# Optimization experiments

Measured on AMD Instinct MI355X. Metric: run time of the kernel, lower is better.

## Reference

```python
import jax, jax.numpy as jnp
import numpy as np

N = 100000      # nodes
E = 3200000     # edges (avg degree 32)
IN_CH = 32
EDGE_DIM = 11
HID = IN_CH + 4 + EDGE_DIM   # 47
OUT = 128


def setup_inputs() -> dict:
    key = jax.random.key(0)
    ks = jax.random.split(key, 10)
    x = jax.random.normal(ks[0], (N, IN_CH), dtype=jnp.float32)
    pos = jax.random.normal(ks[1], (N, 3), dtype=jnp.float32) * 10.0
    nrm = jax.random.normal(ks[2], (N, 3), dtype=jnp.float32)
    normal = nrm / jnp.linalg.norm(nrm, axis=1, keepdims=True)
    # edges with src != dst (avoids degenerate zero-distance point pairs)
    src = jax.random.randint(ks[3], (E,), 0, N)
    off = jax.random.randint(ks[4], (E,), 1, N)
    dst = (src + off) % N
    edge_index = jnp.stack([src, dst], axis=0).astype(jnp.int64)
    edge_attr = jax.random.normal(ks[5], (E, EDGE_DIM), dtype=jnp.float32)
    W1 = jax.random.normal(ks[6], (HID, HID), dtype=jnp.float32) / np.sqrt(HID)
    b1 = jnp.zeros((HID,), dtype=jnp.float32)
    g1 = jnp.ones((HID,), dtype=jnp.float32)
    be1 = jnp.zeros((HID,), dtype=jnp.float32)
    W2 = jax.random.normal(ks[7], (HID, OUT), dtype=jnp.float32) / np.sqrt(HID)
    b2 = jnp.zeros((OUT,), dtype=jnp.float32)
    g2 = jnp.ones((OUT,), dtype=jnp.float32)
    be2 = jnp.zeros((OUT,), dtype=jnp.float32)
    return {"x": x, "pos": pos, "normal": normal, "edge_attr": edge_attr,
            "W1": W1, "b1": b1, "g1": g1, "be1": be1,
            "W2": W2, "b2": b2, "g2": g2, "be2": be2,
            "edge_index": edge_index}


def _angle(v1, v2):
    return jnp.arctan2(jnp.linalg.norm(jnp.cross(v1, v2), axis=1),
                       jnp.sum(v1 * v2, axis=1))


def _layernorm(h, g, b, eps=1e-5):
    mu = jnp.mean(h, axis=-1, keepdims=True)
    var = jnp.var(h, axis=-1, keepdims=True)  # biased, matches torch LayerNorm
    return (h - mu) / jnp.sqrt(var + eps) * g + b


def reference(x, pos, normal, edge_attr, W1, b1, g1, be1, W2, b2, g2, be2, edge_index):
    src, dst = edge_index[0], edge_index[1]  # message flows src(j) -> dst(i)
    pos_i, pos_j = pos[dst], pos[src]
    n_i, n_j = normal[dst], normal[src]
    x_j = x[src]
    pseudo = pos_j - pos_i                                  # [E,3]
    ppf = jnp.stack([jnp.linalg.norm(pseudo, axis=1),
                     _angle(n_i, pseudo),
                     _angle(n_j, pseudo),
                     _angle(n_i, n_j)], axis=1)             # [E,4]
    msg = jnp.concatenate([x_j, ppf, edge_attr], axis=1)    # [E,47]
    # local_nn = MLP([47,47,128]): (Lin->ReLU->LayerNorm->Dropout(eval)) x2
    h = _layernorm(jax.nn.relu(msg @ W1 + b1), g1, be1)     # [E,47]
    h = _layernorm(jax.nn.relu(h @ W2 + b2), g2, be2)       # [E,128]
    out = jax.ops.segment_max(h, dst, num_segments=N)       # scatter-max per target node
    return jnp.where(jnp.isfinite(out), out, 0.0)           # nodes w/o edges -> 0
```

## Files before the change

### kernel.cpp

```cpp
#include <hip/hip_runtime.h>
#include <cstdint>
#include <cstddef>


typedef _Float16 f16x8 __attribute__((ext_vector_type(8)));
typedef _Float16 f16x2 __attribute__((ext_vector_type(2)));
typedef float    f32x4 __attribute__((ext_vector_type(4)));

#define ENC_NEGINF 0x007FFFFFu
#define LDK 64
#define LDH 132

__device__ __forceinline__ int swz(int row, int col) {
    return (col & 7) | ((((col >> 3) ^ row) & 7) << 3);
}

__device__ __forceinline__ unsigned fenc(float f) {
    unsigned u = __float_as_uint(f);
    return (u & 0x80000000u) ? ~u : (u | 0x80000000u);
}

__global__ void init_out_kernel(unsigned* __restrict__ out, int n4) {
    int i = blockIdx.x * blockDim.x + threadIdx.x;
    if (i < n4)
        ((uint4*)out)[i] = make_uint4(ENC_NEGINF, ENC_NEGINF, ENC_NEGINF, ENC_NEGINF);
}

__global__ void finalize_out_kernel(float* __restrict__ out, int n) {
    int i = blockIdx.x * blockDim.x + threadIdx.x;
    if (i < n) {
        unsigned k = __float_as_uint(out[i]);
        float r;
        if (k == ENC_NEGINF) r = 0.0f;
        else {
            unsigned u = (k & 0x80000000u) ? (k ^ 0x80000000u) : ~k;
            r = __uint_as_float(u);
        }
        out[i] = r;
    }
}

__global__ void zero_kernel(int* __restrict__ p, int n) {
    int i = blockIdx.x * blockDim.x + threadIdx.x;
    if (i < n) p[i] = 0;
}

__global__ void hist_kernel(const int* __restrict__ dstI, int* __restrict__ counts, int E) {
    int i = blockIdx.x * blockDim.x + threadIdx.x;
    if (i < E) atomicAdd(&counts[dstI[i]], 1);
}

__global__ __launch_bounds__(1024) void scan_blk(const int* __restrict__ in,
                                                 int* __restrict__ outp,
                                                 int* __restrict__ bsums, int N) {
    __shared__ int wsum[16];
    const int tid = threadIdx.x, lane = tid & 63, wid = tid >> 6;
    int i = blockIdx.x * 1024 + tid;
    int v = (i < N) ? in[i] : 0;
    int incl = v;
#pragma unroll
    for (int m = 1; m < 64; m <<= 1) {
        int t = __shfl_up(incl, m, 64);
        if (lane >= m) incl += t;
    }
    if (lane == 63) wsum[wid] = incl;
    __syncthreads();
    int woff = 0;
#pragma unroll
    for (int k = 0; k < 16; ++k) woff += (k < wid) ? wsum[k] : 0;
    if (i < N) outp[i] = woff + incl - v;
    if (tid == 1023 && bsums != nullptr) bsums[blockIdx.x] = woff + incl;
}

__global__ __launch_bounds__(1024) void scan_add(int* __restrict__ outp,
                                                 const int* __restrict__ bsums, int N) {
    int i = blockIdx.x * 1024 + threadIdx.x;
    if (i < N) outp[i] += bsums[blockIdx.x];
}

__global__ void scatter_kernel(const int* __restrict__ srcI, const int* __restrict__ dstI,
                               int* __restrict__ nextp,
                               int2* __restrict__ se, int* __restrict__ dst_g, int E) {
    int i = blockIdx.x * blockDim.x + threadIdx.x;
    if (i < E) {
        int d = dstI[i];
        int p = atomicAdd(&nextp[d], 1);
        se[p] = make_int2(srcI[i], i);
        dst_g[p] = d;
    }
}

__global__ __launch_bounds__(512, 4) void edge_kernel_csr(
    const float* __restrict__ x,   const float* __restrict__ pos,
    const float* __restrict__ nrm, const float* __restrict__ ea,
    const float* __restrict__ W1,  const float* __restrict__ b1,
    const float* __restrict__ g1,  const float* __restrict__ be1,
    const float* __restrict__ W2,  const float* __restrict__ b2,
    const float* __restrict__ g2,  const float* __restrict__ be2,
    const int2* __restrict__ se,   const int* __restrict__ dst_g,
    unsigned* __restrict__ out, int E, int ntiles, int tilesPerBlock)
{
    __shared__ _Float16 W1t[48][LDK];
    __shared__ _Float16 W2t[128][LDK];
    __shared__ _Float16 msgA[128][LDK];
    __shared__ _Float16 h2w[128][LDH];
    __shared__ int dstL[128];

    const int lane = threadIdx.x & 63;
    const int w    = threadIdx.x >> 6;
    const int c16  = lane & 15;
    const int g    = lane >> 4;
    const int row0 = w * 16;

    for (int i = threadIdx.x; i < 48 * 64; i += 512) {
        int n = i >> 6, k = i & 63;
        W1t[n][swz(n, k)] = (n < 47 && k < 47) ? (_Float16)W1[k * 47 + n] : (_Float16)0.f;
    }
    for (int i = threadIdx.x; i < 128 * 64; i += 512) {
        int n = i >> 6, k = i & 63;
        W2t[n][swz(n, k)] = (k < 47) ? (_Float16)W2[k * 128 + n] : (_Float16)0.f;
    }
    for (int i = threadIdx.x; i < 128 * LDK; i += 512)
        (&msgA[0][0])[i] = (_Float16)0.f;

    float b1v[3], g1v[3], be1v[3];
#pragma unroll
    for (int n = 0; n < 3; ++n) {
        int cc = n * 16 + c16;
        bool vld = cc < 47;
        b1v[n]  = vld ? b1[cc]  : 0.f;
        g1v[n]  = vld ? g1[cc]  : 0.f;
        be1v[n] = vld ? be1[cc] : 0.f;
    }
    float b2v[8], g2v[8], be2v[8];
#pragma unroll
    for (int n = 0; n < 8; ++n) {
        int cc = n * 16 + c16;
        b2v[n] = b2[cc]; g2v[n] = g2[cc]; be2v[n] = be2[cc];
    }
    __syncthreads();

    const int xr = lane >> 2;
    const int xc = (lane & 3) * 8;
    const int eg = lane / 11, ec = lane - eg * 11;
    const bool ea_act  = lane < 44;
    const bool geo_act = lane < 48;

    const int tbeg = blockIdx.x * tilesPerBlock;
    int tend = tbeg + tilesPerBlock;
    if (tend > ntiles) tend = ntiles;

    for (int tile = tbeg; tile < tend; ++tile) {
        const int base = tile * 128 + row0;

        {
            int p = base + xr;
            bool vx = p < E;
            int s = vx ? se[p].x : 0;
            const float4* xp = (const float4*)(x + (size_t)s * 32 + xc);
            float4 xa = xp[0];
            float4 xb = xp[1];

            float eav0 = 0.f, eav1 = 0.f, eav2 = 0.f, eav3 = 0.f;
            if (ea_act) {
                int p0 = base + 0 * 4 + eg, p1 = base + 1 * 4 + eg;
                int p2 = base + 2 * 4 + eg, p3 = base + 3 * 4 + eg;
                int e0 = (p0 < E) ? se[p0].y : 0;
                int e1 = (p1 < E) ? se[p1].y : 0;
                int e2 = (p2 < E) ? se[p2].y : 0;
                int e3 = (p3 < E) ? se[p3].y : 0;
                eav0 = (p0 < E) ? ea[(size_t)e0 * 11 + ec] : 0.f;
                eav1 = (p1 < E) ? ea[(size_t)e1 * 11 + ec] : 0.f;
                eav2 = (p2 < E) ? ea[(size_t)e2 * 11 + ec] : 0.f;
                eav3 = (p3 < E) ? ea[(size_t)e3 * 11 + ec] : 0.f;
            }

            float gpix = 0.f, gpiy = 0.f, gpiz = 0.f;
            float gpjx = 0.f, gpjy = 0.f, gpjz = 0.f;
            float gnix = 0.f, gniy = 0.f, gniz = 0.f;
            float gnjx = 0.f, gnjy = 0.f, gnjz = 0.f;
            int pd = -1;
            if (geo_act) {
                int pg = base + c16;
                bool v = pg < E;
                int s2 = v ? se[pg].x : 0;
                int d2 = v ? dst_g[pg] : 0;
                pd = v ? d2 : -1;
                gpix = pos[d2 * 3 + 0]; gpiy = pos[d2 * 3 + 1]; gpiz = pos[d2 * 3 + 2];
                gpjx = pos[s2 * 3 + 0]; gpjy = pos[s2 * 3 + 1]; gpjz = pos[s2 * 3 + 2];
                gnix = nrm[d2 * 3 + 0]; gniy = nrm[d2 * 3 + 1]; gniz = nrm[d2 * 3 + 2];
                gnjx = nrm[s2 * 3 + 0]; gnjy = nrm[s2 * 3 + 1]; gnjz = nrm[s2 * 3 + 2];
            }

            {
                int r = row0 + xr;
                f16x8 hv;
                hv[0] = (_Float16)(vx ? xa.x : 0.f); hv[1] = (_Float16)(vx ? xa.y : 0.f);
                hv[2] = (_Float16)(vx ? xa.z : 0.f); hv[3] = (_Float16)(vx ? xa.w : 0.f);
                hv[4] = (_Float16)(vx ? xb.x : 0.f); hv[5] = (_Float16)(vx ? xb.y : 0.f);
                hv[6] = (_Float16)(vx ? xb.z : 0.f); hv[7] = (_Float16)(vx ? xb.w : 0.f);
                *(f16x8*)&msgA[r][swz(r, xc)] = hv;
            }
            if (ea_act) {
                int r0 = row0 + 0 * 4 + eg; msgA[r0][swz(r0, 36 + ec)] = (_Float16)eav0;
                int r1 = row0 + 1 * 4 + eg; msgA[r1][swz(r1, 36 + ec)] = (_Float16)eav1;
                int r2 = row0 + 2 * 4 + eg; msgA[r2][swz(r2, 36 + ec)] = (_Float16)eav2;
                int r3 = row0 + 3 * 4 + eg; msgA[r3][swz(r3, 36 + ec)] = (_Float16)eav3;
            }
            if (geo_act) {
                int r = row0 + c16;
                float px = gpjx - gpix, py = gpjy - gpiy, pz = gpjz - gpiz;
                float v1x, v1y, v1z, v2x, v2y, v2z;
                if (g == 0)      { v1x = gnix; v1y = gniy; v1z = gniz; v2x = px;   v2y = py;   v2z = pz; }
                else if (g == 1) { v1x = gnjx; v1y = gnjy; v1z = gnjz; v2x = px;   v2y = py;   v2z = pz; }
                else             { v1x = gnix; v1y = gniy; v1z = gniz; v2x = gnjx; v2y = gnjy; v2z = gnjz; }
                float cx = v1y * v2z - v1z * v2y;
                float cy = v1z * v2x - v1x * v2z;
                float cz = v1x * v2y - v1y * v2x;
                float ang = atan2f(sqrtf(cx * cx + cy * cy + cz * cz),
                                   v1x * v2x + v1y * v2y + v1z * v2z);
                msgA[r][swz(r, 33 + g)] = (_Float16)ang;
                if (g == 0) {
                    msgA[r][swz(r, 32)] = (_Float16)sqrtf(px * px + py * py + pz * pz);
                    dstL[r] = pd;
                }
            }
        }

        f32x4 acc1[3];
#pragma unroll
        for (int n = 0; n < 3; ++n) acc1[n] = (f32x4){0.f, 0.f, 0.f, 0.f};
#pragma unroll
        for (int ks = 0; ks < 2; ++ks) {
            int ar = row0 + c16;
            f16x8 a = *(const f16x8*)&msgA[ar][swz(ar, ks * 32 + g * 8)];
#pragma unroll
            for (int n = 0; n < 3; ++n) {
                int br = n * 16 + c16;
                f16x8 b = *(const f16x8*)&W1t[br][swz(br, ks * 32 + g * 8)];
                acc1[n] = __builtin_amdgcn_mfma_f32_16x16x32_f16(a, b, acc1[n], 0, 0, 0);
            }
        }
#pragma unroll
        for (int q = 0; q < 4; ++q) {
            float t0 = fmaxf(acc1[0][q] + b1v[0], 0.f);
            float t1 = fmaxf(acc1[1][q] + b1v[1], 0.f);
            float t2 = fmaxf(acc1[2][q] + b1v[2], 0.f);
            float s = t0 + t1 + t2;
            float s2 = t0 * t0 + t1 * t1 + t2 * t2;
#pragma unroll
            for (int m = 1; m < 16; m <<= 1) {
                s  += __shfl_xor(s,  m, 64);
                s2 += __shfl_xor(s2, m, 64);
            }
            float mu  = s * (1.f / 47.f);
            float var = s2 * (1.f / 47.f) - mu * mu;
            float rs  = rsqrtf(var + 1e-5f);
            int r = row0 + 4 * g + q;
            msgA[r][swz(r, c16)]      = (_Float16)((t0 - mu) * rs * g1v[0] + be1v[0]);
            msgA[r][swz(r, 16 + c16)] = (_Float16)((t1 - mu) * rs * g1v[1] + be1v[1]);
            msgA[r][swz(r, 32 + c16)] = (_Float16)((t2 - mu) * rs * g1v[2] + be1v[2]);
        }

        f32x4 acc2[8];
#pragma unroll
        for (int n = 0; n < 8; ++n) acc2[n] = (f32x4){0.f, 0.f, 0.f, 0.f};
#pragma unroll
        for (int ks = 0; ks < 2; ++ks) {
            int ar = row0 + c16;
            f16x8 a = *(const f16x8*)&msgA[ar][swz(ar, ks * 32 + g * 8)];
#pragma unroll
            for (int n = 0; n < 8; ++n) {
                int br = n * 16 + c16;
                f16x8 b = *(const f16x8*)&W2t[br][swz(br, ks * 32 + g * 8)];
                acc2[n] = __builtin_amdgcn_mfma_f32_16x16x32_f16(a, b, acc2[n], 0, 0, 0);
            }
        }
#pragma unroll
        for (int q = 0; q < 4; ++q) {
            float t[8];
            float s = 0.f, s2 = 0.f;
#pragma unroll
            for (int n = 0; n < 8; ++n) {
                t[n] = fmaxf(acc2[n][q] + b2v[n], 0.f);
                s += t[n]; s2 += t[n] * t[n];
            }
#pragma unroll
            for (int m = 1; m < 16; m <<= 1) {
                s  += __shfl_xor(s,  m, 64);
                s2 += __shfl_xor(s2, m, 64);
            }
            float mu  = s * (1.f / 128.f);
            float var = s2 * (1.f / 128.f) - mu * mu;
            float rs  = rsqrtf(var + 1e-5f);
            int r = row0 + 4 * g + q;
#pragma unroll
            for (int n = 0; n < 8; ++n) {
                float o = (t[n] - mu) * rs * g2v[n] + be2v[n];
                h2w[r][n * 16 + c16] = (_Float16)o;
            }
        }

        {
            float m0 = -INFINITY, m1 = -INFINITY;
            int segStart = 0;
            int dcur = dstL[row0];
#pragma unroll
            for (int r = 0; r < 16; ++r) {
                f16x2 pk = *(const f16x2*)&h2w[row0 + r][lane * 2];
                m0 = fmaxf(m0, (float)pk[0]);
                m1 = fmaxf(m1, (float)pk[1]);
                int dnext = (r < 15) ? dstL[row0 + r + 1] : -2;
                if (dnext != dcur) {
                    if (dcur >= 0) {
                        unsigned e0 = fenc(m0), e1 = fenc(m1);
                        unsigned* orow = out + (size_t)dcur * 128 + lane * 2;
                        if (segStart > 0 && r < 15) {
                            unsigned long long pk2 =
                                ((unsigned long long)e1 << 32) | (unsigned long long)e0;
                            *(unsigned long long*)orow = pk2;
                        } else {
                            atomicMax(orow,     e0);
                            atomicMax(orow + 1, e1);
                        }
                    }
                    m0 = -INFINITY; m1 = -INFINITY;
                    segStart = r + 1; dcur = dnext;
                }
            }
        }
    }
}

#define LDKF 72
__global__ __launch_bounds__(256) void edge_kernel_atomic(
    const float* __restrict__ x,   const float* __restrict__ pos,
    const float* __restrict__ nrm, const float* __restrict__ ea,
    const float* __restrict__ W1,  const float* __restrict__ b1,
    const float* __restrict__ g1,  const float* __restrict__ be1,
    const float* __restrict__ W2,  const float* __restrict__ b2,
    const float* __restrict__ g2,  const float* __restrict__ be2,
    const int* __restrict__ srcI,  const int* __restrict__ dstI,
    unsigned* __restrict__ out, int E, int ntiles)
{
    __shared__ _Float16 W1t[48][LDKF];
    __shared__ _Float16 W2t[128][LDKF];
    __shared__ _Float16 msgA[64][LDKF];
    __shared__ int dst_s[64];

    const int lane = threadIdx.x & 63;
    const int w    = threadIdx.x >> 6;
    const int c16  = lane & 15;
    const int g    = lane >> 4;

    for (int i = threadIdx.x; i < 48 * 64; i += 256) {
        int n = i >> 6, k = i & 63;
        W1t[n][k] = (n < 47 && k < 47) ? (_Float16)W1[k * 47 + n] : (_Float16)0.f;
    }
    for (int i = threadIdx.x; i < 128 * 64; i += 256) {
        int n = i >> 6, k = i & 63;
        W2t[n][k] = (k < 47) ? (_Float16)W2[k * 128 + n] : (_Float16)0.f;
    }
    for (int i = threadIdx.x; i < 64 * LDKF; i += 256)
        (&msgA[0][0])[i] = (_Float16)0.f;

    float b1v[3], g1v[3], be1v[3];
#pragma unroll
    for (int n = 0; n < 3; ++n) {
        int cc = n * 16 + c16;
        bool vld = cc < 47;
        b1v[n]  = vld ? b1[cc]  : 0.f;
        g1v[n]  = vld ? g1[cc]  : 0.f;
        be1v[n] = vld ? be1[cc] : 0.f;
    }
    float b2v[8], g2v[8], be2v[8];
#pragma unroll
    for (int n = 0; n < 8; ++n) {
        int cc = n * 16 + c16;
        b2v[n] = b2[cc]; g2v[n] = g2[cc]; be2v[n] = be2[cc];
    }
    __syncthreads();

    for (int tile = blockIdx.x; tile < ntiles; tile += gridDim.x) {
        const int base = tile * 64 + w * 16;
        const int row0 = w * 16;
#pragma unroll
        for (int i = 0; i < 8; ++i) {
            int el = i * 2 + (lane >> 5);
            int e  = base + el;
            int c  = lane & 31;
            float v = 0.f;
            if (e < E) v = x[(size_t)srcI[e] * 32 + c];
            msgA[row0 + el][c] = (_Float16)v;
        }
        if (lane < 44) {
            int eg = lane / 11, c = lane - eg * 11;
#pragma unroll
            for (int i = 0; i < 4; ++i) {
                int el = i * 4 + eg;
                int e  = base + el;
                float v = 0.f;
                if (e < E) v = ea[(size_t)e * 11 + c];
                msgA[row0 + el][36 + c] = (_Float16)v;
            }
        }
        if (lane < 48) {
            int el = c16;
            int e  = base + el;
            int s = 0, d = 0;
            bool vld = e < E;
            if (vld) { s = srcI[e]; d = dstI[e]; }
            float pix = pos[d * 3 + 0], piy = pos[d * 3 + 1], piz = pos[d * 3 + 2];
            float pjx = pos[s * 3 + 0], pjy = pos[s * 3 + 1], pjz = pos[s * 3 + 2];
            float nix = nrm[d * 3 + 0], niy = nrm[d * 3 + 1], niz = nrm[d * 3 + 2];
            float njx = nrm[s * 3 + 0], njy = nrm[s * 3 + 1], njz = nrm[s * 3 + 2];
            float px = pjx - pix, py = pjy - piy, pz = pjz - piz;
            float v1x, v1y, v1z, v2x, v2y, v2z;
            if (g == 0)      { v1x = nix; v1y = niy; v1z = niz; v2x = px;  v2y = py;  v2z = pz;  }
            else if (g == 1) { v1x = njx; v1y = njy; v1z = njz; v2x = px;  v2y = py;  v2z = pz;  }
        else             { v1x = nix; v1y = niy; v1z = niz; v2x = njx; v2y = njy; v2z = njz; }
            float cx = v1y * v2z - v1z * v2y;
            float cy = v1z * v2x - v1x * v2z;
            float cz = v1x * v2y - v1y * v2x;
            float ang = atan2f(sqrtf(cx * cx + cy * cy + cz * cz),
                               v1x * v2x + v1y * v2y + v1z * v2z);
            msgA[row0 + el][33 + g] = (_Float16)ang;
            if (g == 0) {
                msgA[row0 + el][32] = (_Float16)sqrtf(px * px + py * py + pz * pz);
                dst_s[row0 + el] = vld ? d : -1;
            }
        }

        f32x4 acc1[3];
#pragma unroll
        for (int n = 0; n < 3; ++n) acc1[n] = (f32x4){0.f, 0.f, 0.f, 0.f};
#pragma unroll
        for (int ks = 0; ks < 2; ++ks) {
            f16x8 a = *(const f16x8*)&msgA[row0 + c16][ks * 32 + g * 8];
#pragma unroll
            for (int n = 0; n < 3; ++n) {
                f16x8 b = *(const f16x8*)&W1t[n * 16 + c16][ks * 32 + g * 8];
                acc1[n] = __builtin_amdgcn_mfma_f32_16x16x32_f16(a, b, acc1[n], 0, 0, 0);
            }
        }
#pragma unroll
        for (int q = 0; q < 4; ++q) {
            float t0 = fmaxf(acc1[0][q] + b1v[0], 0.f);
            float t1 = fmaxf(acc1[1][q] + b1v[1], 0.f);
            float t2 = fmaxf(acc1[2][q] + b1v[2], 0.f);
            float s = t0 + t1 + t2;
            float s2 = t0 * t0 + t1 * t1 + t2 * t2;
#pragma unroll
            for (int m = 1; m < 16; m <<= 1) {
                s  += __shfl_xor(s,  m, 64);
                s2 += __shfl_xor(s2, m, 64);
            }
            float mu  = s * (1.f / 47.f);
            float var = s2 * (1.f / 47.f) - mu * mu;
            float rs  = rsqrtf(var + 1e-5f);
            int r = row0 + 4 * g + q;
            msgA[r][c16]      = (_Float16)((t0 - mu) * rs * g1v[0] + be1v[0]);
            msgA[r][16 + c16] = (_Float16)((t1 - mu) * rs * g1v[1] + be1v[1]);
            msgA[r][32 + c16] = (_Float16)((t2 - mu) * rs * g1v[2] + be1v[2]);
        }

        f32x4 acc2[8];
#pragma unroll
        for (int n = 0; n < 8; ++n) acc2[n] = (f32x4){0.f, 0.f, 0.f, 0.f};
#pragma unroll
        for (int ks = 0; ks < 2; ++ks) {
            f16x8 a = *(const f16x8*)&msgA[row0 + c16][ks * 32 + g * 8];
#pragma unroll
            for (int n = 0; n < 8; ++n) {
                f16x8 b = *(const f16x8*)&W2t[n * 16 + c16][ks * 32 + g * 8];
                acc2[n] = __builtin_amdgcn_mfma_f32_16x16x32_f16(a, b, acc2[n], 0, 0, 0);
            }
        }
        int4 dd = *(const int4*)&dst_s[row0 + 4 * g];
#pragma unroll
        for (int q = 0; q < 4; ++q) {
            float t[8];
            float s = 0.f, s2 = 0.f;
#pragma unroll
            for (int n = 0; n < 8; ++n) {
                t[n] = fmaxf(acc2[n][q] + b2v[n], 0.f);
                s += t[n]; s2 += t[n] * t[n];
            }
#pragma unroll
            for (int m = 1; m < 16; m <<= 1) {
                s  += __shfl_xor(s,  m, 64);
                s2 += __shfl_xor(s2, m, 64);
            }
            float mu  = s * (1.f / 128.f);
            float var = s2 * (1.f / 128.f) - mu * mu;
            float rs  = rsqrtf(var + 1e-5f);
            int d = (&dd.x)[q];
            if (d >= 0) {
                unsigned* orow = out + (size_t)d * 128u;
#pragma unroll
                for (int n = 0; n < 8; ++n) {
                    float o = (t[n] - mu) * rs * g2v[n] + be2v[n];
                    atomicMax(orow + n * 16 + c16, fenc(o));
                }
            }
        }
    }
}

extern "C" void kernel_launch(void* const* d_in, const int* in_sizes, int n_in,
                              void* d_out, int out_size, void* d_ws, size_t ws_size,
                              hipStream_t stream) {
    const float* x   = (const float*)d_in[0];
    const float* pos = (const float*)d_in[1];
    const float* nrm = (const float*)d_in[2];
    const float* ea  = (const float*)d_in[3];
    const float* W1  = (const float*)d_in[4];
    const float* b1  = (const float*)d_in[5];
    const float* g1  = (const float*)d_in[6];
    const float* be1 = (const float*)d_in[7];
    const float* W2  = (const float*)d_in[8];
    const float* b2  = (const float*)d_in[9];
    const float* g2  = (const float*)d_in[10];
    const float* be2 = (const float*)d_in[11];
    const int*   idx = (const int*)d_in[12];

    const int N = in_sizes[0] / 32;
    const int E = in_sizes[3] / 11;
    const int* srcI = idx;
    const int* dstI = idx + E;

    unsigned* outU = (unsigned*)d_out;
    const int n = N * 128;

    init_out_kernel<<<(n / 4 + 255) / 256, 256, 0, stream>>>(outU, n / 4);

    const int nb = (N + 1023) / 1024;
    const size_t needed = (size_t)E * 8 + (size_t)(2LL * N + E + nb) * 4;

    if (ws_size >= needed) {
        int2* se     = (int2*)d_ws;
        int*  counts = (int*)(se + E);
        int*  nextp  = counts + N;
        int*  dst_g  = nextp + N;
        int*  bsums  = dst_g + E;

        zero_kernel<<<(N + 255) / 256, 256, 0, stream>>>(counts, N);
        hist_kernel<<<(E + 255) / 256, 256, 0, stream>>>(dstI, counts, E);
        scan_blk<<<nb, 1024, 0, stream>>>(counts, nextp, bsums, N);
        scan_blk<<<1, 1024, 0, stream>>>(bsums, bsums, (int*)nullptr, nb);
        scan_add<<<nb, 1024, 0, stream>>>(nextp, bsums, N);
        scatter_kernel<<<(E + 255) / 256, 256, 0, stream>>>(srcI, dstI, nextp,
                                                            se, dst_g, E);

        const int ntiles = (E + 127) / 128;
        int grid = ntiles < 512 ? ntiles : 512;
        int tpb  = (ntiles + grid - 1) / grid;
        edge_kernel_csr<<<grid, 512, 0, stream>>>(x, pos, nrm, ea,
                                                  W1, b1, g1, be1,
                                                  W2, b2, g2, be2,
                                                  se, dst_g,
                                                  outU, E, ntiles, tpb);
    } else {
        const int ntiles = (E + 63) / 64;
        int grid = ntiles < 4096 ? ntiles : 4096;
        edge_kernel_atomic<<<grid, 256, 0, stream>>>(x, pos, nrm, ea,
                                                     W1, b1, g1, be1,
                                                     W2, b2, g2, be2,
                                                     srcI, dstI, outU, E, ntiles);
    }

    finalize_out_kernel<<<(n + 255) / 256, 256, 0, stream>>>((float*)d_out, n);
}
```

Measured before the change: 919.5 us.

## Pack LayerNorm2 epilogue and max-reduce in fp16, fold scan_add, vectorize finalize

The second LayerNorm's normalize/affine step now runs on packed fp16 pairs via cvt_pkrtz, and the per-segment max reduction compares in fp16 instead of converting to fp32. The scan_add kernel is removed: scatter_kernel adds the block-level prefix sum when it computes positions. finalize_out uses uint4/float4 vector loads and stores. Together these cut ALU work in the edge epilogue and trim launches and memory traffic. The cost is lower precision in the LayerNorm output, since values are now rounded toward zero in fp16, and -65504 is used as the identity in place of -inf.

```diff
diff --git a/kernel.cpp b/kernel.cpp
--- a/kernel.cpp
+++ b/kernel.cpp
@@ -18,6 +18,17 @@
 __device__ __forceinline__ unsigned fenc(float f) {
     unsigned u = __float_as_uint(f);
     return (u & 0x80000000u) ? ~u : (u | 0x80000000u);
+}
+
+__device__ __forceinline__ float fdec(unsigned k) {
+    if (k == ENC_NEGINF) return 0.0f;
+    unsigned u = (k & 0x80000000u) ? (k ^ 0x80000000u) : ~k;
+    return __uint_as_float(u);
+}
+
+__device__ __forceinline__ f16x2 pkrtz(float a, float b) {
+    auto p = __builtin_amdgcn_cvt_pkrtz(a, b);
+    return __builtin_bit_cast(f16x2, p);
 }
 
 __global__ void init_out_kernel(unsigned* __restrict__ out, int n4) {
@@ -26,17 +37,13 @@
         ((uint4*)out)[i] = make_uint4(ENC_NEGINF, ENC_NEGINF, ENC_NEGINF, ENC_NEGINF);
 }
 
-__global__ void finalize_out_kernel(float* __restrict__ out, int n) {
+__global__ void finalize_out_kernel(float* __restrict__ out, int n4) {
     int i = blockIdx.x * blockDim.x + threadIdx.x;
-    if (i < n) {
-        unsigned k = __float_as_uint(out[i]);
-        float r;
-        if (k == ENC_NEGINF) r = 0.0f;
-        else {
-            unsigned u = (k & 0x80000000u) ? (k ^ 0x80000000u) : ~k;
-            r = __uint_as_float(u);
-        }
-        out[i] = r;
+    if (i < n4) {
+        uint4 k = ((const uint4*)out)[i];
+        float4 r;
+        r.x = fdec(k.x); r.y = fdec(k.y); r.z = fdec(k.z); r.w = fdec(k.w);
+        ((float4*)out)[i] = r;
     }
 }
 
@@ -72,19 +79,13 @@
     if (tid == 1023 && bsums != nullptr) bsums[blockIdx.x] = woff + incl;
 }
 
-__global__ __launch_bounds__(1024) void scan_add(int* __restrict__ outp,
-                                                 const int* __restrict__ bsums, int N) {
-    int i = blockIdx.x * 1024 + threadIdx.x;
-    if (i < N) outp[i] += bsums[blockIdx.x];
-}
-
 __global__ void scatter_kernel(const int* __restrict__ srcI, const int* __restrict__ dstI,
-                               int* __restrict__ nextp,
+                               int* __restrict__ nextp, const int* __restrict__ bsums,
                                int2* __restrict__ se, int* __restrict__ dst_g, int E) {
     int i = blockIdx.x * blockDim.x + threadIdx.x;
     if (i < E) {
         int d = dstI[i];
-        int p = atomicAdd(&nextp[d], 1);
+        int p = bsums[d >> 10] + atomicAdd(&nextp[d], 1);
         se[p] = make_int2(srcI[i], i);
         dst_g[p] = d;
     }
@@ -132,11 +133,16 @@
         g1v[n]  = vld ? g1[cc]  : 0.f;
         be1v[n] = vld ? be1[cc] : 0.f;
     }
-    float b2v[8], g2v[8], be2v[8];
-#pragma unroll
-    for (int n = 0; n < 8; ++n) {
-        int cc = n * 16 + c16;
-        b2v[n] = b2[cc]; g2v[n] = g2[cc]; be2v[n] = be2[cc];
+    float b2v[8];
+    f16x2 g2pk[4], be2pk[4];
+#pragma unroll
+    for (int n = 0; n < 8; ++n) b2v[n] = b2[n * 16 + c16];
+#pragma unroll
+    for (int h = 0; h < 4; ++h) {
+        g2pk[h][0]  = (_Float16)g2[(2 * h) * 16 + c16];
+        g2pk[h][1]  = (_Float16)g2[(2 * h + 1) * 16 + c16];
+        be2pk[h][0] = (_Float16)be2[(2 * h) * 16 + c16];
+        be2pk[h][1] = (_Float16)be2[(2 * h + 1) * 16 + c16];
     }
     __syncthreads();
 
@@ -294,26 +300,33 @@
             float var = s2 * (1.f / 128.f) - mu * mu;
             float rs  = rsqrtf(var + 1e-5f);
             int r = row0 + 4 * g + q;
-#pragma unroll
-            for (int n = 0; n < 8; ++n) {
-                float o = (t[n] - mu) * rs * g2v[n] + be2v[n];
-                h2w[r][n * 16 + c16] = (_Float16)o;
+            f16x2 apk = pkrtz(rs, rs);
+            f16x2 cpk = pkrtz(-mu * rs, -mu * rs);
+#pragma unroll
+            for (int h = 0; h < 4; ++h) {
+                f16x2 tpk = pkrtz(t[2 * h], t[2 * h + 1]);
+                f16x2 z   = tpk * apk + cpk;
+                f16x2 hvp = z * g2pk[h] + be2pk[h];
+                h2w[r][(2 * h) * 16 + c16]     = hvp[0];
+                h2w[r][(2 * h + 1) * 16 + c16] = hvp[1];
             }
         }
 
         {
-            float m0 = -INFINITY, m1 = -INFINITY;
+            f16x2 mneg; mneg[0] = mneg[1] = (_Float16)(-65504.f);
+            f16x2 mx = mneg;
             int segStart = 0;
             int dcur = dstL[row0];
 #pragma unroll
             for (int r = 0; r < 16; ++r) {
                 f16x2 pk = *(const f16x2*)&h2w[row0 + r][lane * 2];
-                m0 = fmaxf(m0, (float)pk[0]);
-                m1 = fmaxf(m1, (float)pk[1]);
+                mx[0] = (pk[0] > mx[0]) ? pk[0] : mx[0];
+                mx[1] = (pk[1] > mx[1]) ? pk[1] : mx[1];
                 int dnext = (r < 15) ? dstL[row0 + r + 1] : -2;
                 if (dnext != dcur) {
                     if (dcur >= 0) {
-                        unsigned e0 = fenc(m0), e1 = fenc(m1);
+                        unsigned e0 = fenc((float)mx[0]);
+                        unsigned e1 = fenc((float)mx[1]);
                         unsigned* orow = out + (size_t)dcur * 128 + lane * 2;
                         if (segStart > 0 && r < 15) {
                             unsigned long long pk2 =
@@ -324,7 +337,7 @@
                             atomicMax(orow + 1, e1);
                         }
                     }
-                    m0 = -INFINITY; m1 = -INFINITY;
+                    mx = mneg;
                     segStart = r + 1; dcur = dnext;
                 }
             }
@@ -418,7 +431,7 @@
             float v1x, v1y, v1z, v2x, v2y, v2z;
             if (g == 0)      { v1x = nix; v1y = niy; v1z = niz; v2x = px;  v2y = py;  v2z = pz;  }
             else if (g == 1) { v1x = njx; v1y = njy; v1z = njz; v2x = px;  v2y = py;  v2z = pz;  }
-        else             { v1x = nix; v1y = niy; v1z = niz; v2x = njx; v2y = njy; v2z = njz; }
+            else             { v1x = nix; v1y = niy; v1z = niz; v2x = njx; v2y = njy; v2z = njz; }
             float cx = v1y * v2z - v1z * v2y;
             float cy = v1z * v2x - v1x * v2z;
             float cz = v1x * v2y - v1y * v2x;
@@ -548,8 +561,7 @@
         hist_kernel<<<(E + 255) / 256, 256, 0, stream>>>(dstI, counts, E);
         scan_blk<<<nb, 1024, 0, stream>>>(counts, nextp, bsums, N);
         scan_blk<<<1, 1024, 0, stream>>>(bsums, bsums, (int*)nullptr, nb);
-        scan_add<<<nb, 1024, 0, stream>>>(nextp, bsums, N);
-        scatter_kernel<<<(E + 255) / 256, 256, 0, stream>>>(srcI, dstI, nextp,
+        scatter_kernel<<<(E + 255) / 256, 256, 0, stream>>>(srcI, dstI, nextp, bsums,
                                                             se, dst_g, E);
 
         const int ntiles = (E + 127) / 128;
@@ -569,5 +581,5 @@
                                                      srcI, dstI, outU, E, ntiles);
     }
 
-    finalize_out_kernel<<<(n + 255) / 256, 256, 0, stream>>>((float*)d_out, n);
-}
+    finalize_out_kernel<<<(n / 4 + 255) / 256, 256, 0, stream>>>((float*)d_out, n / 4);
+}
```

Result: faster. 852.8 us (-7.3%).
